# Performance work log

Measured on AMD Instinct MI355X. Metric: run time of the kernel, lower is better.

## Reference

```python
import jax, jax.numpy as jnp
import numpy as np

NUM_EMBEDDINGS = 512
EMBEDDING_DIM = 64
COMMITMENT_COST = 0.25


def setup_inputs() -> dict:
    key = jax.random.key(0)
    k1, k2 = jax.random.split(key)
    inputs = jax.random.normal(k1, (256, 2048, EMBEDDING_DIM), dtype=jnp.float32)
    # Glorot uniform for (num_embeddings, embedding_dim)
    limit = np.sqrt(6.0 / (NUM_EMBEDDINGS + EMBEDDING_DIM)).astype(np.float32)
    embeddings = jax.random.uniform(k2, (NUM_EMBEDDINGS, EMBEDDING_DIM),
                                    dtype=jnp.float32, minval=-limit, maxval=limit)
    return {"inputs": inputs, "embeddings": embeddings}


def reference(inputs, embeddings):
    D = embeddings.shape[1]
    flat = inputs.reshape(-1, D)  # [N, D]
    # squared L2 distances via the expanded form (matches the TF code exactly)
    distances = (jnp.sum(flat * flat, axis=1, keepdims=True)
                 + jnp.sum(embeddings * embeddings, axis=1)
                 - 2.0 * flat @ embeddings.T)  # [N, K]
    encoding_indices = jnp.argmin(distances, axis=1)  # [N]
    # direct gather (same math as one-hot matmul, avoids the dense [N,K] matmul)
    quantized = embeddings[encoding_indices].reshape(inputs.shape)
    commitment_loss = COMMITMENT_COST * jnp.mean(
        (jax.lax.stop_gradient(quantized) - inputs) ** 2)
    embedding_loss = jnp.mean((jax.lax.stop_gradient(inputs) - quantized) ** 2)
    # straight-through estimator
    quantized_st = inputs + jax.lax.stop_gradient(quantized - inputs)
    return quantized_st, commitment_loss, embedding_loss
```

## Files before the change

kernel.cpp:

```cpp
#include <hip/hip_runtime.h>
#include <cfloat>

typedef _Float16 f16;
typedef f16 f16x8 __attribute__((ext_vector_type(8)));
typedef float f32x4 __attribute__((ext_vector_type(4)));

#define NTOK (256 * 2048)
#define DDIM 64
#define K 512
#define TPB 256
#define GRID_MAIN 4096
#define GRID_RES  2048
#define THR 1.0e-3f

#define WS_NEEDED 681984

__device__ __forceinline__ float sq_tree64(const float* __restrict__ x) {
    float g0, g1, g2, g3, g4, g5, g6, g7;
#define GRP(G, dst)                                                                      \
    do {                                                                                 \
        float p0 = __fmul_rn(x[8 * G + 0], x[8 * G + 0]);                                \
        float p1 = __fmul_rn(x[8 * G + 1], x[8 * G + 1]);                                \
        float p2 = __fmul_rn(x[8 * G + 2], x[8 * G + 2]);                                \
        float p3 = __fmul_rn(x[8 * G + 3], x[8 * G + 3]);                                \
        float p4 = __fmul_rn(x[8 * G + 4], x[8 * G + 4]);                                \
        float p5 = __fmul_rn(x[8 * G + 5], x[8 * G + 5]);                                \
        float p6 = __fmul_rn(x[8 * G + 6], x[8 * G + 6]);                                \
        float p7 = __fmul_rn(x[8 * G + 7], x[8 * G + 7]);                                \
        dst = __fadd_rn(__fadd_rn(__fadd_rn(p0, p1), __fadd_rn(p2, p3)),                 \
                        __fadd_rn(__fadd_rn(p4, p5), __fadd_rn(p6, p7)));                \
    } while (0)
    GRP(0, g0); GRP(1, g1); GRP(2, g2); GRP(3, g3);
    GRP(4, g4); GRP(5, g5); GRP(6, g6); GRP(7, g7);
#undef GRP
    return __fadd_rn(__fadd_rn(__fadd_rn(g0, g1), __fadd_rn(g2, g3)),
                     __fadd_rn(__fadd_rn(g4, g5), __fadd_rn(g6, g7)));
}

__global__ void vq_prep_kernel(const float* __restrict__ emb, f16* __restrict__ pack,
                               float* __restrict__ se) {
    const int b = blockIdx.x, l = threadIdx.x;
    if (b < 128) {
        const int split = b & 1;
        const int ds = (b >> 1) & 1;
        const int ct = b >> 2;
        const int code = ct * 16 + (l & 15);
        const int dbase = ds * 32 + (l >> 4) * 8;
        const float* src = emb + (size_t)code * DDIM + dbase;
        f16x8 v;
#pragma unroll
        for (int j = 0; j < 8; ++j) {
            float t = -2.0f * src[j];
            f16 h = (f16)t;
            if (split == 0) v[j] = h;
            else            v[j] = (f16)((t - (float)h) * 2048.0f);
        }
        *(f16x8*)(pack + (size_t)b * 512 + (size_t)l * 8) = v;
    } else {
        const int k = (b - 128) * 64 + l;
        se[k] = sq_tree64(emb + (size_t)k * DDIM);
    }
}

__global__ void vq_senorm_kernel(const float* __restrict__ emb,
                                 float* __restrict__ se) {
    int k = threadIdx.x;
    se[k] = sq_tree64(emb + (size_t)k * DDIM);
}

#define STAGE_SUPER(buf, s)                                                              \
    do {                                                                                 \
        const char* _g = (const char*)pack + (size_t)(s) * 16384 + (size_t)w * 4096 +    \
                         (size_t)l * 16;                                                 \
        char* _d = (char*)(&Bbuf[(buf)][0]) + (size_t)w * 4096 + (size_t)l * 16;         \
        __builtin_amdgcn_global_load_lds(                                                \
            (const __attribute__((address_space(1))) unsigned int*)_g,                   \
            (__attribute__((address_space(3))) unsigned int*)_d, 16, 0, 0);              \
        __builtin_amdgcn_global_load_lds(                                                \
            (const __attribute__((address_space(1))) unsigned int*)(_g + 1024),          \
            (__attribute__((address_space(3))) unsigned int*)(_d + 1024), 16, 0, 0);     \
        __builtin_amdgcn_global_load_lds(                                                \
            (const __attribute__((address_space(1))) unsigned int*)(_g + 2048),          \
            (__attribute__((address_space(3))) unsigned int*)(_d + 2048), 16, 0, 0);     \
        __builtin_amdgcn_global_load_lds(                                                \
            (const __attribute__((address_space(1))) unsigned int*)(_g + 3072),          \
            (__attribute__((address_space(3))) unsigned int*)(_d + 3072), 16, 0, 0);     \
    } while (0)

__global__ __launch_bounds__(TPB, 4) void vq_main_kernel(
        const float* __restrict__ xg, const float* __restrict__ emb,
        const f16* __restrict__ pack, const float* __restrict__ se,
        float* __restrict__ out, float* __restrict__ bsum,
        unsigned char* __restrict__ flags) {
    __shared__ f16x8 Bbuf[2][1024];
    __shared__ int   kw_lds[4][2][16];
    __shared__ float dw_lds[4][2][16];
    __shared__ float wave_part[4];

    const int tid = threadIdx.x;
    const int w  = tid >> 6;
    const int l  = tid & 63;
    const int lg = l >> 4;
    const int lc = l & 15;
    const size_t base = ((size_t)blockIdx.x * 4 + w) * 32;

    f16x8 Ah[2][2], Al[2][2];
    float sx[2];
#pragma unroll
    for (int i = 0; i < 2; ++i) {
        const float* xp = xg + (base + i * 16 + lc) * DDIM + lg * 8;
        float acc = 0.f;
#pragma unroll
        for (int ds = 0; ds < 2; ++ds) {
            float4 u0 = *(const float4*)(xp + ds * 32);
            float4 u1 = *(const float4*)(xp + ds * 32 + 4);
            float v[8] = {u0.x, u0.y, u0.z, u0.w, u1.x, u1.y, u1.z, u1.w};
            f16x8 h, lo;
#pragma unroll
            for (int j = 0; j < 8; ++j) {
                f16 hh = (f16)v[j];
                h[j]  = hh;
                lo[j] = (f16)((v[j] - (float)hh) * 2048.0f);
                acc = __fmaf_rn(v[j], v[j], acc);
            }
            Ah[i][ds] = h; Al[i][ds] = lo;
        }
        sx[i] = acc;
    }
#pragma unroll
    for (int i = 0; i < 2; ++i) {
        sx[i] += __shfl_xor(sx[i], 16, 64);
        sx[i] += __shfl_xor(sx[i], 32, 64);
    }

    float dmin[2][4], dsec[2][4];
    int   kmin[2][4];
#pragma unroll
    for (int i = 0; i < 2; ++i)
#pragma unroll
        for (int r = 0; r < 4; ++r) { dmin[i][r] = FLT_MAX; dsec[i][r] = FLT_MAX; kmin[i][r] = 0; }

    const int rot = blockIdx.x & 7;
    const float* sebase = se + lc;
    float cs0 = sebase[rot * 64], cs1 = sebase[rot * 64 + 16],
          cs2 = sebase[rot * 64 + 32], cs3 = sebase[rot * 64 + 48];
    STAGE_SUPER(0, rot);

    for (int sp = 0; sp < 8; ++sp) {
        const int cur = sp & 1;
        const int s  = (sp + rot) & 7;

        asm volatile("s_waitcnt vmcnt(0)" ::: "memory");
        __builtin_amdgcn_s_barrier();

        float ns0 = 0.f, ns1 = 0.f, ns2 = 0.f, ns3 = 0.f;
        if (sp < 7) {
            STAGE_SUPER(cur ^ 1, (sp + 1 + rot) & 7);
            const int sn = ((sp + 1 + rot) & 7) * 64;
            ns0 = sebase[sn]; ns1 = sebase[sn + 16];
            ns2 = sebase[sn + 32]; ns3 = sebase[sn + 48];
        }

#pragma unroll
        for (int cl = 0; cl < 4; ++cl) {
            const int ct = s * 4 + cl;
            const int code = ct * 16 + lc;
            const float sek = (cl == 0) ? cs0 : (cl == 1) ? cs1 : (cl == 2) ? cs2 : cs3;
            f16x8 Bh0 = Bbuf[cur][cl * 256 +   0 + l];
            f16x8 Bl0 = Bbuf[cur][cl * 256 +  64 + l];
            f16x8 Bh1 = Bbuf[cur][cl * 256 + 128 + l];
            f16x8 Bl1 = Bbuf[cur][cl * 256 + 192 + l];
#pragma unroll
            for (int i = 0; i < 2; ++i) {
                f32x4 am = {sek, sek, sek, sek};
                f32x4 ac = {0.f, 0.f, 0.f, 0.f};
                am = __builtin_amdgcn_mfma_f32_16x16x32_f16(Ah[i][0], Bh0, am, 0, 0, 0);
                am = __builtin_amdgcn_mfma_f32_16x16x32_f16(Ah[i][1], Bh1, am, 0, 0, 0);
                ac = __builtin_amdgcn_mfma_f32_16x16x32_f16(Al[i][0], Bh0, ac, 0, 0, 0);
                ac = __builtin_amdgcn_mfma_f32_16x16x32_f16(Al[i][1], Bh1, ac, 0, 0, 0);
                ac = __builtin_amdgcn_mfma_f32_16x16x32_f16(Ah[i][0], Bl0, ac, 0, 0, 0);
                ac = __builtin_amdgcn_mfma_f32_16x16x32_f16(Ah[i][1], Bl1, ac, 0, 0, 0);
#pragma unroll
                for (int r = 0; r < 4; ++r) {
                    float v = __fmaf_rn(ac[r], 4.8828125e-4f, am[r]);
                    bool lt = v < dmin[i][r];
                    dsec[i][r] = __builtin_amdgcn_fmed3f(v, dmin[i][r], dsec[i][r]);
                    dmin[i][r] = fminf(v, dmin[i][r]);
                    kmin[i][r] = lt ? code : kmin[i][r];
                }
            }
        }
        cs0 = ns0; cs1 = ns1; cs2 = ns2; cs3 = ns3;
    }

#pragma unroll
    for (int i = 0; i < 2; ++i)
#pragma unroll
        for (int r = 0; r < 4; ++r) {
#pragma unroll
            for (int off = 1; off <= 8; off <<= 1) {
                float dvm = __shfl_xor(dmin[i][r], off, 64);
                int   kvm = __shfl_xor(kmin[i][r], off, 64);
                float dvs = __shfl_xor(dsec[i][r], off, 64);
                bool take = dvm < dmin[i][r];
                float lose = take ? dmin[i][r] : dvm;
                if (take) { dmin[i][r] = dvm; kmin[i][r] = kvm; }
                dsec[i][r] = fminf(fminf(dsec[i][r], dvs), lose);
            }
        }

    if (lc == 0) {
#pragma unroll
        for (int i = 0; i < 2; ++i)
#pragma unroll
            for (int r = 0; r < 4; ++r) {
                int fl = (dsec[i][r] <= dmin[i][r] + THR) ? 1 : 0;
                kw_lds[w][i][lg * 4 + r] = kmin[i][r] | (fl << 31);
                dw_lds[w][i][lg * 4 + r] = dmin[i][r];
                flags[base + i * 16 + lg * 4 + r] = (unsigned char)fl;
            }
    }
    __syncthreads();

#pragma unroll
    for (int m = 0; m < 8; ++m) {
        const int row = m * 4 + (l >> 4);
        const int kwv = kw_lds[w][row >> 4][row & 15] & 0x7fffffff;
        f32x4 vsrc = ((const f32x4*)(emb + (size_t)kwv * DDIM))[lc];
        __builtin_nontemporal_store(vsrc, (f32x4*)(out + (base + row) * DDIM) + lc);
    }

    float lp = 0.f;
    if (l < 16) {
        int k0 = kw_lds[w][0][l], k1 = kw_lds[w][1][l];
        float t0 = (k0 < 0) ? 0.f : __fadd_rn(sx[0], dw_lds[w][0][l]);
        float t1 = (k1 < 0) ? 0.f : __fadd_rn(sx[1], dw_lds[w][1][l]);
        lp = __fadd_rn(t0, t1);
    }
#pragma unroll
    for (int off = 32; off >= 1; off >>= 1) lp += __shfl_down(lp, off, 64);
    if (l == 0) wave_part[w] = lp;
    __syncthreads();
    if (tid == 0) {
        bsum[blockIdx.x] = __fadd_rn(__fadd_rn(wave_part[0], wave_part[1]),
                                     __fadd_rn(wave_part[2], wave_part[3]));
    }
}

__global__ __launch_bounds__(TPB) void vq_rescore_kernel(
        const float* __restrict__ xg, const float* __restrict__ emb,
        const float* __restrict__ se, const unsigned char* __restrict__ flags,
        float* __restrict__ out, float* __restrict__ bsum2) {
    __shared__ int   list[TPB];
    __shared__ float lp_tok[TPB];
    __shared__ int   wcnt[4];
    __shared__ float x_lds[4][DDIM];
    __shared__ float red[TPB / 64];

    const int tid = threadIdx.x;
    const int w = tid >> 6, lane = tid & 63;
    const size_t tok0 = (size_t)blockIdx.x * TPB;
    const int flag = flags[tok0 + tid] != 0;

    lp_tok[tid] = 0.f;
    unsigned long long bal = __ballot(flag);
    if (lane == 0) wcnt[w] = __popcll(bal);
    __syncthreads();
    int off = 0;
#pragma unroll
    for (int ww = 0; ww < 4; ++ww) off += (ww < w) ? wcnt[ww] : 0;
    const int cnt = wcnt[0] + wcnt[1] + wcnt[2] + wcnt[3];
    if (flag) list[off + __popcll(bal & ((1ULL << lane) - 1))] = tid;
    __syncthreads();

    for (int i = w; i < cnt; i += 4) {
        const int tloc = __builtin_amdgcn_readfirstlane(list[i]);
        const size_t tok = tok0 + tloc;

        if (lane < 16)
            ((float4*)&x_lds[w][0])[lane] = ((const float4*)(xg + tok * DDIM))[lane];
        asm volatile("s_waitcnt vmcnt(0) lgkmcnt(0)" ::: "memory");

        const float sx = sq_tree64(&x_lds[w][0]);

        float dmin = FLT_MAX;
        int   kmin = K;
#pragma unroll
        for (int c = 0; c < 8; ++c) {
            const int k = c * 64 + lane;
            const float* ek = emb + (size_t)k * DDIM;
            const float sek = se[k];
            float a0 = 0.f, a1 = 0.f, a2 = 0.f, a3 = 0.f;
#pragma unroll
            for (int j = 0; j < DDIM; j += 4) {
                float4 e4 = *(const float4*)(ek + j);
                a0 = __fmaf_rn(x_lds[w][j + 0], e4.x, a0);
                a1 = __fmaf_rn(x_lds[w][j + 1], e4.y, a1);
                a2 = __fmaf_rn(x_lds[w][j + 2], e4.z, a2);
                a3 = __fmaf_rn(x_lds[w][j + 3], e4.w, a3);
            }
            float dot = __fadd_rn(__fadd_rn(a0, a1), __fadd_rn(a2, a3));
            float d = __fsub_rn(__fadd_rn(sx, sek), __fmul_rn(2.0f, dot));
            if (d < dmin) { dmin = d; kmin = k; }
        }
#pragma unroll
        for (int o = 1; o <= 32; o <<= 1) {
            float dv = __shfl_xor(dmin, o, 64);
            int   kv = __shfl_xor(kmin, o, 64);
            if (dv < dmin || (dv == dmin && kv < kmin)) { dmin = dv; kmin = kv; }
        }

        {
            const float4* esrc = (const float4*)(emb + (size_t)kmin * DDIM);
            if (lane < 16)
                ((float4*)(out + tok * DDIM))[lane] = esrc[lane];
            float lp = 0.f;
#pragma unroll
            for (int q = 0; q < DDIM / 4; ++q) {
                float4 v = esrc[q];
                float d0 = __fsub_rn(v.x, x_lds[w][4 * q + 0]); lp = __fmaf_rn(d0, d0, lp);
                float d1 = __fsub_rn(v.y, x_lds[w][4 * q + 1]); lp = __fmaf_rn(d1, d1, lp);
                float d2 = __fsub_rn(v.z, x_lds[w][4 * q + 2]); lp = __fmaf_rn(d2, d2, lp);
                float d3 = __fsub_rn(v.w, x_lds[w][4 * q + 3]); lp = __fmaf_rn(d3, d3, lp);
            }
            if (lane == 0) lp_tok[tloc] = lp;
        }
    }
    __syncthreads();

    float lp = lp_tok[tid];
#pragma unroll
    for (int o = 32; o >= 1; o >>= 1) lp += __shfl_down(lp, o, 64);
    if (lane == 0) red[w] = lp;
    __syncthreads();
    if (tid == 0) {
        bsum2[blockIdx.x] = __fadd_rn(__fadd_rn(red[0], red[1]),
                                      __fadd_rn(red[2], red[3]));
    }
}

__global__ __launch_bounds__(TPB) void vq_main_f32_kernel(
        const float* __restrict__ xg, const float* __restrict__ emb,
        const float* __restrict__ se, float* __restrict__ out,
        float* __restrict__ bsum) {
    __shared__ int   lds_kmin[TPB];
    __shared__ float lds_red[TPB / 64];
    const int tid = threadIdx.x;
    const size_t tok = (size_t)blockIdx.x * TPB + tid;
    float x[DDIM];
    {
        const float4* xg4 = (const float4*)(xg + tok * DDIM);
#pragma unroll
        for (int q = 0; q < DDIM / 4; ++q) {
            float4 v = xg4[q];
            x[4 * q + 0] = v.x; x[4 * q + 1] = v.y;
            x[4 * q + 2] = v.z; x[4 * q + 3] = v.w;
        }
    }
    const float sx = sq_tree64(x);
    float dmin = FLT_MAX; int kmin = 0;
    for (int k = 0; k < K; ++k) {
        const float* ek = emb + (size_t)k * DDIM;
        const float sek = se[k];
        float a0 = 0.f, a1 = 0.f, a2 = 0.f, a3 = 0.f;
#pragma unroll
        for (int j = 0; j < DDIM; j += 4) {
            a0 = __fmaf_rn(x[j + 0], ek[j + 0], a0);
            a1 = __fmaf_rn(x[j + 1], ek[j + 1], a1);
            a2 = __fmaf_rn(x[j + 2], ek[j + 2], a2);
            a3 = __fmaf_rn(x[j + 3], ek[j + 3], a3);
        }
        float dot = __fadd_rn(__fadd_rn(a0, a1), __fadd_rn(a2, a3));
        float d = __fsub_rn(__fadd_rn(sx, sek), __fmul_rn(2.0f, dot));
        if (d < dmin) { dmin = d; kmin = k; }
    }
    float lp = 0.f;
    {
        const float4* e4 = (const float4*)(emb + (size_t)kmin * DDIM);
#pragma unroll
        for (int q = 0; q < DDIM / 4; ++q) {
            float4 v = e4[q];
            float d0 = __fsub_rn(v.x, x[4 * q + 0]); lp = __fmaf_rn(d0, d0, lp);
            float d1 = __fsub_rn(v.y, x[4 * q + 1]); lp = __fmaf_rn(d1, d1, lp);
            float d2 = __fsub_rn(v.z, x[4 * q + 2]); lp = __fmaf_rn(d2, d2, lp);
            float d3 = __fsub_rn(v.w, x[4 * q + 3]); lp = __fmaf_rn(d3, d3, lp);
        }
    }
    lds_kmin[tid] = kmin;
#pragma unroll
    for (int off = 32; off >= 1; off >>= 1) lp += __shfl_down(lp, off, 64);
    if ((tid & 63) == 0) lds_red[tid >> 6] = lp;
    __syncthreads();
    if (tid == 0) {
        float s = lds_red[0];
#pragma unroll
        for (int w = 1; w < TPB / 64; ++w) s = __fadd_rn(s, lds_red[w]);
        bsum[blockIdx.x] = s;
    }
    {
        const float4* emb4 = (const float4*)emb;
        float4* out4 = (float4*)out + (size_t)blockIdx.x * (TPB * DDIM / 4);
#pragma unroll
        for (int it = 0; it < (TPB * DDIM / 4) / TPB; ++it) {
            int m = it * TPB + tid;
            int t = m >> 4, q = m & 15;
            out4[m] = emb4[(size_t)lds_kmin[t] * 16 + q];
        }
    }
}

__global__ void vq_loss_kernel(const float* __restrict__ bsum, int nb1,
                               const float* __restrict__ bsum2, int nb2,
                               float* __restrict__ out_losses) {
    __shared__ float red[256];
    int tid = threadIdx.x;
    float s = 0.f;
    for (int i = tid; i < nb1; i += 256) s = __fadd_rn(s, bsum[i]);
    for (int i = tid; i < nb2; i += 256) s = __fadd_rn(s, bsum2[i]);
    red[tid] = s;
    __syncthreads();
    for (int off = 128; off >= 1; off >>= 1) {
        if (tid < off) red[tid] = __fadd_rn(red[tid], red[tid + off]);
        __syncthreads();
    }
    if (tid == 0) {
        float mean = red[0] / (float)((long long)NTOK * DDIM);
        out_losses[0] = 0.25f * mean;
        out_losses[1] = mean;
    }
}

extern "C" void kernel_launch(void* const* d_in, const int* in_sizes, int n_in,
                              void* d_out, int out_size, void* d_ws, size_t ws_size,
                              hipStream_t stream) {
    const float* xg  = (const float*)d_in[0];
    const float* emb = (const float*)d_in[1];
    float* out = (float*)d_out;
    char* ws = (char*)d_ws;

    if (ws_size >= (size_t)WS_NEEDED) {
        f16*   pack  = (f16*)ws;
        float* se    = (float*)(ws + 131072);
        float* bsum  = (float*)(ws + 133120);
        float* bsum2 = (float*)(ws + 149504);
        unsigned char* flags = (unsigned char*)(ws + 157696);

        vq_prep_kernel<<<136, 64, 0, stream>>>(emb, pack, se);
        vq_main_kernel<<<GRID_MAIN, TPB, 0, stream>>>(xg, emb, pack, se, out, bsum, flags);
        vq_rescore_kernel<<<GRID_RES, TPB, 0, stream>>>(xg, emb, se, flags, out, bsum2);
        vq_loss_kernel<<<1, 256, 0, stream>>>(bsum, GRID_MAIN, bsum2, GRID_RES,
                                              out + (size_t)NTOK * DDIM);
    } else {
        float* se   = (float*)ws;
        float* bsum = se + K;
        vq_senorm_kernel<<<1, K, 0, stream>>>(emb, se);
        vq_main_f32_kernel<<<NTOK / TPB, TPB, 0, stream>>>(xg, emb, se, out, bsum);
        vq_loss_kernel<<<1, 256, 0, stream>>>(bsum, NTOK / TPB, bsum, 0,
                                              out + (size_t)NTOK * DDIM);
    }
}
```

Before: 190.8 us.

## Switch codebook staging to triple-buffered half-size stages and cache norms in LDS

Replaces the double-buffered 16KB codebook stages with three 8KB buffers, so each of the 16 smaller stages is prefetched two steps ahead using a partial vmcnt wait. Codebook squared norms are loaded once into shared memory instead of being prefetched from global memory per stage. The aim is to hide global-to-LDS latency better and reduce register pressure. The cost is twice as many barriers and extra LDS use (about 26KB in total), which may affect occupancy.

```diff
diff --git a/kernel.cpp b/kernel.cpp
--- a/kernel.cpp
+++ b/kernel.cpp
@@ -68,23 +68,17 @@
     se[k] = sq_tree64(emb + (size_t)k * DDIM);
 }
 
-#define STAGE_SUPER(buf, s)                                                              \
+#define STAGE3(buf, s)                                                                   \
     do {                                                                                 \
-        const char* _g = (const char*)pack + (size_t)(s) * 16384 + (size_t)w * 4096 +    \
+        const char* _g = (const char*)pack + (size_t)(s) * 8192 + (size_t)w * 1024 +     \
                          (size_t)l * 16;                                                 \
-        char* _d = (char*)(&Bbuf[(buf)][0]) + (size_t)w * 4096 + (size_t)l * 16;         \
+        char* _d = (char*)(&Bbuf[(buf)][0]) + (size_t)w * 1024 + (size_t)l * 16;         \
         __builtin_amdgcn_global_load_lds(                                                \
             (const __attribute__((address_space(1))) unsigned int*)_g,                   \
             (__attribute__((address_space(3))) unsigned int*)_d, 16, 0, 0);              \
         __builtin_amdgcn_global_load_lds(                                                \
-            (const __attribute__((address_space(1))) unsigned int*)(_g + 1024),          \
-            (__attribute__((address_space(3))) unsigned int*)(_d + 1024), 16, 0, 0);     \
-        __builtin_amdgcn_global_load_lds(                                                \
-            (const __attribute__((address_space(1))) unsigned int*)(_g + 2048),          \
-            (__attribute__((address_space(3))) unsigned int*)(_d + 2048), 16, 0, 0);     \
-        __builtin_amdgcn_global_load_lds(                                                \
-            (const __attribute__((address_space(1))) unsigned int*)(_g + 3072),          \
-            (__attribute__((address_space(3))) unsigned int*)(_d + 3072), 16, 0, 0);     \
+            (const __attribute__((address_space(1))) unsigned int*)(_g + 4096),          \
+            (__attribute__((address_space(3))) unsigned int*)(_d + 4096), 16, 0, 0);     \
     } while (0)
 
 __global__ __launch_bounds__(TPB, 4) void vq_main_kernel(
@@ -92,7 +86,8 @@
         const f16* __restrict__ pack, const float* __restrict__ se,
         float* __restrict__ out, float* __restrict__ bsum,
         unsigned char* __restrict__ flags) {
-    __shared__ f16x8 Bbuf[2][1024];
+    __shared__ f16x8 Bbuf[3][512];
+    __shared__ float se_lds[K];
     __shared__ int   kw_lds[4][2][16];
     __shared__ float dw_lds[4][2][16];
     __shared__ float wave_part[4];
@@ -104,6 +99,9 @@
     const int lc = l & 15;
     const size_t base = ((size_t)blockIdx.x * 4 + w) * 32;
 
+    se_lds[tid] = se[tid];
+    se_lds[tid + 256] = se[tid + 256];
+
     f16x8 Ah[2][2], Al[2][2];
     float sx[2];
 #pragma unroll
@@ -140,32 +138,27 @@
 #pragma unroll
         for (int r = 0; r < 4; ++r) { dmin[i][r] = FLT_MAX; dsec[i][r] = FLT_MAX; kmin[i][r] = 0; }
 
-    const int rot = blockIdx.x & 7;
-    const float* sebase = se + lc;
-    float cs0 = sebase[rot * 64], cs1 = sebase[rot * 64 + 16],
-          cs2 = sebase[rot * 64 + 32], cs3 = sebase[rot * 64 + 48];
-    STAGE_SUPER(0, rot);
-
-    for (int sp = 0; sp < 8; ++sp) {
-        const int cur = sp & 1;
-        const int s  = (sp + rot) & 7;
-
-        asm volatile("s_waitcnt vmcnt(0)" ::: "memory");
+    __syncthreads();
+
+    const int rot = blockIdx.x & 15;
+    STAGE3(0, rot);
+    STAGE3(1, (1 + rot) & 15);
+
+    for (int sp = 0; sp < 16; ++sp) {
+        const int cur = sp % 3;
+        const int s  = (sp + rot) & 15;
+
+        if (sp < 15) asm volatile("s_waitcnt vmcnt(2)" ::: "memory");
+        else         asm volatile("s_waitcnt vmcnt(0)" ::: "memory");
         __builtin_amdgcn_s_barrier();
 
-        float ns0 = 0.f, ns1 = 0.f, ns2 = 0.f, ns3 = 0.f;
-        if (sp < 7) {
-            STAGE_SUPER(cur ^ 1, (sp + 1 + rot) & 7);
-            const int sn = ((sp + 1 + rot) & 7) * 64;
-            ns0 = sebase[sn]; ns1 = sebase[sn + 16];
-            ns2 = sebase[sn + 32]; ns3 = sebase[sn + 48];
-        }
-
-#pragma unroll
-        for (int cl = 0; cl < 4; ++cl) {
-            const int ct = s * 4 + cl;
+        if (sp < 14) STAGE3((sp + 2) % 3, (sp + 2 + rot) & 15);
+
+#pragma unroll
+        for (int cl = 0; cl < 2; ++cl) {
+            const int ct = s * 2 + cl;
             const int code = ct * 16 + lc;
-            const float sek = (cl == 0) ? cs0 : (cl == 1) ? cs1 : (cl == 2) ? cs2 : cs3;
+            const float sek = se_lds[ct * 16 + lc];
             f16x8 Bh0 = Bbuf[cur][cl * 256 +   0 + l];
             f16x8 Bl0 = Bbuf[cur][cl * 256 +  64 + l];
             f16x8 Bh1 = Bbuf[cur][cl * 256 + 128 + l];
@@ -190,7 +183,6 @@
                 }
             }
         }
-        cs0 = ns0; cs1 = ns1; cs2 = ns2; cs3 = ns3;
     }
 
 #pragma unroll
```

New measurement: 190.5 us, median of 2. Within noise of the previous version (-0.2%).
